# Optimization experiments

Hardware: AMD Instinct MI355X
Metric: run time of the kernel (lower is better)

Reference implementation:

```python
import jax, jax.numpy as jnp
import numpy as np

D_MODEL = 256   # per-head dim in this module
N_HEAD = 8
B, S = 4, 2048
NEG_INF = -1e9  # large negative in place of -inf for numerical safety


def setup_inputs() -> dict:
    key = jax.random.key(0)
    ks = jax.random.split(key, 8)
    d, h = D_MODEL, N_HEAD
    sc = 1.0 / np.sqrt(d)
    return {
        "Q": jax.random.normal(ks[0], (B, S, d), jnp.float32),
        "mask": jax.random.randint(ks[1], (B, S), 0, 2, jnp.int32),
        "WQ_w": jax.random.normal(ks[2], (h * d, d), jnp.float32) * sc,
        "WQ_b": jnp.zeros((h * d,), jnp.float32),
        "WK_w": jax.random.normal(ks[3], (h * d, d), jnp.float32) * sc,
        "WK_b": jnp.zeros((h * d,), jnp.float32),
        "WV_w": jax.random.normal(ks[4], (h * d, d), jnp.float32) * sc,
        "WV_b": jnp.zeros((h * d,), jnp.float32),
        "WO_w": jax.random.normal(ks[5], (d, h * d), jnp.float32) * sc,
        "WO_b": jnp.zeros((d,), jnp.float32),
        "ln_g": jnp.ones((d,), jnp.float32),
        "ln_b": jnp.zeros((d,), jnp.float32),
    }


def reference(Q, mask, WQ_w, WQ_b, WK_w, WK_b, WV_w, WV_b, WO_w, WO_b, ln_g, ln_b):
    b, s, d = Q.shape
    h = N_HEAD
    # projections (torch Linear: x @ W.T + b), split into heads: [b, h, s, d]
    q = (Q @ WQ_w.T + WQ_b).reshape(b, s, h, d).transpose(0, 2, 1, 3)
    k = (Q @ WK_w.T + WK_b).reshape(b, s, h, d).transpose(0, 2, 1, 3)
    v = (Q @ WV_w.T + WV_b).reshape(b, s, h, d).transpose(0, 2, 1, 3)
    # scaled dot-product scores [b, h, q, k]
    scores = jnp.einsum('bhqd,bhkd->bhqk', q, k) / jnp.sqrt(jnp.asarray(d, Q.dtype))
    key_mask = (mask != 0)[:, None, None, :]  # [b,1,1,k]
    scores = jnp.where(key_mask, scores, NEG_INF)
    alpha = jax.nn.softmax(scores, axis=-1)
    out = jnp.einsum('bhqk,bhkd->bhqd', alpha, v)
    out = out.transpose(0, 2, 1, 3).reshape(b, s, h * d)
    out = out @ WO_w.T + WO_b + Q  # dropout is identity in eval
    # LayerNorm over last dim
    mu = out.mean(-1, keepdims=True)
    var = out.var(-1, keepdims=True)
    return (out - mu) / jnp.sqrt(var + 1e-5) * ln_g + ln_b
```

## Files before the change

kernel.cpp:

```cpp
#include <hip/hip_runtime.h>
#include <cstddef>
#include <cstdint>

#define SQ 2048
#define DH 256
#define NH 8
#define BATCH 4
#define MROWS (BATCH*SQ)
#define HID (NH*DH)

typedef __attribute__((ext_vector_type(8)))  short bf16x8;
typedef __attribute__((ext_vector_type(16))) float f32x16;

typedef __attribute__((address_space(1))) const unsigned char gbuf_t;
typedef __attribute__((address_space(3))) unsigned char lbuf_t;

__device__ __forceinline__ void gl_lds16(const void* g, void* l) {
  __builtin_amdgcn_global_load_lds((gbuf_t*)g, (lbuf_t*)l, 16, 0, 0);
}

__device__ __forceinline__ unsigned short f2bf(float f) {
  unsigned u = __float_as_uint(f);
  unsigned r = (u + 0x7FFFu + ((u >> 16) & 1u)) >> 16;
  return (unsigned short)r;
}
__device__ __forceinline__ unsigned pk2(float a, float b) {
  return (unsigned)f2bf(a) | ((unsigned)f2bf(b) << 16);
}
__device__ __forceinline__ f32x16 zero16() {
  f32x16 v;
#pragma unroll
  for (int i = 0; i < 16; ++i) v[i] = 0.0f;
  return v;
}

__global__ void __launch_bounds__(256) cvt_kernel(
    const float* __restrict__ X,  const float* __restrict__ Wq,
    const float* __restrict__ Wk, const float* __restrict__ Wv,
    const float* __restrict__ Wo,
    unsigned short* __restrict__ Xb,  unsigned short* __restrict__ Wqb,
    unsigned short* __restrict__ Wkb, unsigned short* __restrict__ Wvb,
    unsigned short* __restrict__ Wob)
{
  int bid = blockIdx.x;
  const float* src; unsigned short* dst; size_t off;
  if      (bid < 512) { src = X;  dst = Xb;  off = (size_t)bid * 4096; }
  else if (bid < 640) { src = Wq; dst = Wqb; off = (size_t)(bid - 512) * 4096; }
  else if (bid < 768) { src = Wk; dst = Wkb; off = (size_t)(bid - 640) * 4096; }
  else if (bid < 896) { src = Wv; dst = Wvb; off = (size_t)(bid - 768) * 4096; }
  else                { src = Wo; dst = Wob; off = (size_t)(bid - 896) * 4096; }
  int tid = threadIdx.x;
#pragma unroll
  for (int k = 0; k < 4; ++k) {
    size_t idx = off + ((size_t)k * 256 + tid) * 4;
    float4 v = *(const float4*)(src + idx);
    uint2 o; o.x = pk2(v.x, v.y); o.y = pk2(v.z, v.w);
    *(uint2*)(dst + idx) = o;
  }
}

__global__ void __launch_bounds__(256) qkv_kernel(
    const unsigned short* __restrict__ Xbf,
    const unsigned short* __restrict__ Wqb,
    const unsigned short* __restrict__ Wkb,
    const unsigned short* __restrict__ Wvb,
    const float* __restrict__ bq, const float* __restrict__ bk, const float* __restrict__ bv,
    unsigned short* __restrict__ q_ws, unsigned short* __restrict__ k_ws,
    unsigned short* __restrict__ vt_ws)
{
  __shared__ unsigned char TA[65536];
  __shared__ unsigned char TB[65536];
  const int tid = threadIdx.x, w = tid >> 6, l = tid & 63;
  const int h = l >> 5, t = l & 31;
  const int wm = w >> 1, wn = w & 1;
  const int z = blockIdx.z;
  const int m0 = (z == 2) ? blockIdx.y * 128 : blockIdx.x * 128;
  const int n0 = (z == 2) ? blockIdx.x * 128 : blockIdx.y * 128;
  const unsigned short* Asrc = (z == 2) ? Wvb : Xbf;
  const unsigned short* Bsrc = (z == 0) ? Wqb : (z == 1) ? Wkb : Xbf;

  const int rowo = l >> 5;
  const int bin  = (l & 31) * 16;
#pragma unroll
  for (int i2 = 0; i2 < 16; ++i2) {
    int i = 16 * w + i2;
    int row = 2 * i + rowo;
    gl_lds16((const unsigned char*)(Asrc + (size_t)(m0 + row) * 256) + (bin ^ ((row & 15) << 4)),
             &TA[i * 1024]);
  }
#pragma unroll
  for (int i2 = 0; i2 < 16; ++i2) {
    int i = 16 * w + i2;
    int row = 2 * i + rowo;
    gl_lds16((const unsigned char*)(Bsrc + (size_t)(n0 + row) * 256) + (bin ^ ((row & 15) << 4)),
             &TB[i * 1024]);
  }
  __syncthreads();

  f32x16 acc00 = zero16(), acc01 = zero16(), acc10 = zero16(), acc11 = zero16();
  const int swz = (t & 15) << 4;
#pragma unroll
  for (int kc = 0; kc < 16; ++kc) {
    int kb = (32 * kc + 16 * h) ^ swz;
    bf16x8 a0 = *(const bf16x8*)&TA[(size_t)(64 * wm + t) * 512 + kb];
    bf16x8 a1 = *(const bf16x8*)&TA[(size_t)(64 * wm + 32 + t) * 512 + kb];
    bf16x8 b0 = *(const bf16x8*)&TB[(size_t)(64 * wn + t) * 512 + kb];
    bf16x8 b1 = *(const bf16x8*)&TB[(size_t)(64 * wn + 32 + t) * 512 + kb];
    acc00 = __builtin_amdgcn_mfma_f32_32x32x16_bf16(a0, b0, acc00, 0, 0, 0);
    acc01 = __builtin_amdgcn_mfma_f32_32x32x16_bf16(a0, b1, acc01, 0, 0, 0);
    acc10 = __builtin_amdgcn_mfma_f32_32x32x16_bf16(a1, b0, acc10, 0, 0, 0);
    acc11 = __builtin_amdgcn_mfma_f32_32x32x16_bf16(a1, b1, acc11, 0, 0, 0);
  }

  if (z < 2) {
    unsigned short* outp = z ? k_ws : q_ws;
    const float* bias = z ? bk : bq;
    float bn0 = bias[n0 + 64 * wn + t];
    float bn1 = bias[n0 + 64 * wn + 32 + t];
#pragma unroll
    for (int mt = 0; mt < 2; ++mt) {
#pragma unroll
      for (int nt = 0; nt < 2; ++nt) {
        int n = n0 + 64 * wn + 32 * nt + t;
        int headn = n >> 8, d = n & 255;
        float bb = nt ? bn1 : bn0;
        const f32x16& A = (mt == 0) ? (nt == 0 ? acc00 : acc01) : (nt == 0 ? acc10 : acc11);
#pragma unroll
        for (int r = 0; r < 16; ++r) {
          int m = m0 + 64 * wm + 32 * mt + (r & 3) + 8 * (r >> 2) + 4 * h;
          int batch = m >> 11, s = m & 2047;
          outp[(((size_t)batch * NH + headn) * SQ + s) * DH + d] = f2bf(A[r] + bb);
        }
      }
    }
  } else {
#pragma unroll
    for (int mt = 0; mt < 2; ++mt) {
#pragma unroll
      for (int r = 0; r < 16; ++r) {
        int j = m0 + 64 * wm + 32 * mt + (r & 3) + 8 * (r >> 2) + 4 * h;
        float bj = bv[j];
        int headj = j >> 8, jl = j & 255;
#pragma unroll
        for (int nt = 0; nt < 2; ++nt) {
          int sall = n0 + 64 * wn + 32 * nt + t;
          int batch = sall >> 11, ss = sall & 2047;
          const f32x16& A = (mt == 0) ? (nt == 0 ? acc00 : acc01) : (nt == 0 ? acc10 : acc11);
          vt_ws[((size_t)batch * NH + headj) * DH * SQ + (size_t)jl * SQ + ss] = f2bf(A[r] + bj);
        }
      }
    }
  }
}

__global__ void __launch_bounds__(512, 2) attn_kernel(
    const unsigned short* __restrict__ q_ws,
    const unsigned short* __restrict__ k_ws,
    const unsigned short* __restrict__ vt_ws,
    const int* __restrict__ mask,
    unsigned short* __restrict__ o_ws)
{
  __shared__ unsigned char KT[2][32768];
  __shared__ unsigned char VT[2][32768];
  __shared__ float MB[2048];

  const int tid = threadIdx.x, w = tid >> 6, l = tid & 63;
  const int h = l >> 5, t = l & 31;
  const int bid = blockIdx.x;
  const int xcd = bid & 7, slot = bid >> 3;
  const int bh = xcd * 4 + (slot >> 3);
  const int qt = slot & 7;
  const int b = bh >> 3, head = bh & 7;
  const int q0 = qt * 256;

  {
    const int* mrow = mask + b * SQ;
    for (int i = tid; i < SQ; i += 512) MB[i] = mrow[i] ? 0.0f : -1e9f;
  }

  const unsigned short* kplane = k_ws + (size_t)bh * SQ * DH;
  const unsigned short* vplane = vt_ws + (size_t)bh * DH * SQ;

  bf16x8 qf[16];
  {
    const unsigned short* qb = q_ws + ((size_t)bh * SQ + (q0 + 32 * w + t)) * DH + 8 * h;
#pragma unroll
    for (int kc = 0; kc < 16; ++kc) qf[kc] = *(const bf16x8*)(qb + 16 * kc);
  }

  const int krow_o = l >> 5, kcol = (l & 31) * 16;
  const int vrow_o = l >> 3, vcol = (l & 7) * 16;

  {
#pragma unroll
    for (int i = 0; i < 4; ++i) {
      int j = 4 * w + i;
      int row = 2 * j + krow_o;
      gl_lds16((const unsigned char*)(kplane + (size_t)row * DH) + (kcol ^ ((row & 15) << 4)),
               &KT[0][j * 1024]);
    }
#pragma unroll
    for (int i = 0; i < 4; ++i) {
      int j = 4 * w + i;
      int row = 8 * j + vrow_o;
      gl_lds16((const unsigned char*)(vplane + (size_t)row * SQ) + (vcol ^ ((row & 7) << 4)),
               &VT[0][j * 1024]);
    }
  }
  __syncthreads();

  f32x16 o[8];
#pragma unroll
  for (int i = 0; i < 8; ++i) o[i] = zero16();
  float m_run = -3.0e38f, l_run = 0.0f;

  const int swzK = (t & 15) << 4;
  const int swzV = (t & 7) << 4;

  int cur = 0;
  for (int kb = 0; kb < SQ; kb += 64) {
    const int nxt = cur ^ 1;
    if (kb + 64 < SQ) {
#pragma unroll
      for (int i = 0; i < 4; ++i) {
        int j = 4 * w + i;
        int row = 2 * j + krow_o;
        gl_lds16((const unsigned char*)(kplane + (size_t)(kb + 64 + row) * DH) + (kcol ^ ((row & 15) << 4)),
                 &KT[nxt][j * 1024]);
      }
#pragma unroll
      for (int i = 0; i < 4; ++i) {
        int j = 4 * w + i;
        int row = 8 * j + vrow_o;
        gl_lds16((const unsigned char*)(vplane + (size_t)row * SQ + kb + 64) + (vcol ^ ((row & 7) << 4)),
                 &VT[nxt][j * 1024]);
      }
    }

    f32x16 sa0 = zero16(), sa1 = zero16();
    __builtin_amdgcn_s_setprio(1);
#pragma unroll
    for (int kc = 0; kc < 16; ++kc) {
      int kbb = (32 * kc + 16 * h) ^ swzK;
      bf16x8 a0 = *(const bf16x8*)&KT[cur][(size_t)t * 512 + kbb];
      bf16x8 a1 = *(const bf16x8*)&KT[cur][(size_t)(32 + t) * 512 + kbb];
      sa0 = __builtin_amdgcn_mfma_f32_32x32x16_bf16(a0, qf[kc], sa0, 0, 0, 0);
      sa1 = __builtin_amdgcn_mfma_f32_32x32x16_bf16(a1, qf[kc], sa1, 0, 0, 0);
    }
    __builtin_amdgcn_s_setprio(0);

    float tm = -3.0e38f;
    const float* mbp = &MB[kb + 4 * h];
#pragma unroll
    for (int r = 0; r < 16; ++r) {
      int kl = (r & 3) + 8 * (r >> 2);
      sa0[r] = sa0[r] * 0.0625f + mbp[kl];
      sa1[r] = sa1[r] * 0.0625f + mbp[32 + kl];
      tm = fmaxf(tm, fmaxf(sa0[r], sa1[r]));
    }
    tm = fmaxf(tm, __shfl_xor(tm, 32, 64));
    float m_new = fmaxf(m_run, tm);
    float rf = __expf(m_run - m_new);
    m_run = m_new;
    float ls = 0.0f;
#pragma unroll
    for (int r = 0; r < 16; ++r) {
      sa0[r] = __expf(sa0[r] - m_new);
      sa1[r] = __expf(sa1[r] - m_new);
      ls += sa0[r] + sa1[r];
    }
    ls += __shfl_xor(ls, 32, 64);
    l_run = l_run * rf + ls;

#pragma unroll
    for (int r = 0; r < 16; ++r) {
      float rr = __shfl(rf, (r & 3) + 8 * (r >> 2) + 4 * h, 64);
#pragma unroll
      for (int db = 0; db < 8; ++db) o[db][r] *= rr;
    }

    bf16x8 pa[4];
#pragma unroll
    for (int ks = 0; ks < 4; ++ks) {
      const f32x16& P = (ks < 2) ? sa0 : sa1;
      const int base = 8 * (ks & 1);
      unsigned lo0 = pk2(P[base + 0], P[base + 1]);
      unsigned lo1 = pk2(P[base + 2], P[base + 3]);
      unsigned hi0 = pk2(P[base + 4], P[base + 5]);
      unsigned hi1 = pk2(P[base + 6], P[base + 7]);
      unsigned s0 = h ? lo0 : hi0;
      unsigned s1 = h ? lo1 : hi1;
      unsigned x0 = (unsigned)__shfl_xor((int)s0, 32, 64);
      unsigned x1 = (unsigned)__shfl_xor((int)s1, 32, 64);
      union { unsigned u[4]; bf16x8 v; } pu;
      pu.u[0] = h ? x0 : lo0;
      pu.u[1] = h ? x1 : lo1;
      pu.u[2] = h ? hi0 : x0;
      pu.u[3] = h ? hi1 : x1;
      pa[ks] = pu.v;
    }

    __builtin_amdgcn_s_setprio(1);
#pragma unroll
    for (int db = 0; db < 8; ++db) {
#pragma unroll
      for (int ks = 0; ks < 4; ++ks) {
        bf16x8 bv = *(const bf16x8*)&VT[cur][(size_t)(32 * db + t) * 128 + ((32 * ks + 16 * h) ^ swzV)];
        o[db] = __builtin_amdgcn_mfma_f32_32x32x16_bf16(pa[ks], bv, o[db], 0, 0, 0);
      }
    }
    __builtin_amdgcn_s_setprio(0);

    __syncthreads();
    cur = nxt;
  }

  float linv = 1.0f / l_run;
  unsigned short* ob = o_ws + (size_t)b * SQ * HID + (size_t)head * DH;
#pragma unroll
  for (int r = 0; r < 16; ++r) {
    int rowr = (r & 3) + 8 * (r >> 2) + 4 * h;
    float li = __shfl(linv, rowr, 64);
    int s = q0 + 32 * w + rowr;
    unsigned short* orow = ob + (size_t)s * HID;
#pragma unroll
    for (int db = 0; db < 8; ++db)
      orow[32 * db + t] = f2bf(o[db][r] * li);
  }
}

__global__ void __launch_bounds__(256) oproj_kernel(
    const unsigned short* __restrict__ Abf,
    const unsigned short* __restrict__ Wob,
    float* __restrict__ tmp)
{
  __shared__ unsigned char TA[8192];
  __shared__ unsigned char TB[16384];
  const int tid = threadIdx.x, w = tid >> 6, l = tid & 63;
  const int h = l >> 5, t = l & 31;
  const int wm = w >> 1, wn = w & 1;
  const int m0 = blockIdx.x * 64, n0 = blockIdx.y * 128;
  const int arow_o = l >> 3, ab_in = (l & 7) * 16;
  const int swz = (t & 7) << 4;

  f32x16 acc0 = zero16(), acc1 = zero16();
  for (int chunk = 0; chunk < 32; ++chunk) {
    __syncthreads();
#pragma unroll
    for (int i2 = 0; i2 < 2; ++i2) {
      int i = 2 * w + i2;
      int row = 8 * i + arow_o;
      gl_lds16((const unsigned char*)(Abf + (size_t)(m0 + row) * HID + chunk * 64) + (ab_in ^ ((row & 7) << 4)),
               &TA[i * 1024]);
    }
#pragma unroll
    for (int i2 = 0; i2 < 4; ++i2) {
      int i = 4 * w + i2;
      int row = 8 * i + arow_o;
      gl_lds16((const unsigned char*)(Wob + (size_t)(n0 + row) * HID + chunk * 64) + (ab_in ^ ((row & 7) << 4)),
               &TB[i * 1024]);
    }
    __syncthreads();
#pragma unroll
    for (int kc = 0; kc < 4; ++kc) {
      int kbb = (32 * kc + 16 * h) ^ swz;
      bf16x8 a  = *(const bf16x8*)&TA[(size_t)(32 * wm + t) * 128 + kbb];
      bf16x8 b0 = *(const bf16x8*)&TB[(size_t)(64 * wn + t) * 128 + kbb];
      bf16x8 b1 = *(const bf16x8*)&TB[(size_t)(64 * wn + 32 + t) * 128 + kbb];
      acc0 = __builtin_amdgcn_mfma_f32_32x32x16_bf16(a, b0, acc0, 0, 0, 0);
      acc1 = __builtin_amdgcn_mfma_f32_32x32x16_bf16(a, b1, acc1, 0, 0, 0);
    }
  }
#pragma unroll
  for (int nt = 0; nt < 2; ++nt) {
    const f32x16& A = nt ? acc1 : acc0;
    int n = n0 + 64 * wn + 32 * nt + t;
#pragma unroll
    for (int r = 0; r < 16; ++r) {
      int m = m0 + 32 * wm + (r & 3) + 8 * (r >> 2) + 4 * h;
      tmp[(size_t)m * DH + n] = A[r];
    }
  }
}

__global__ void __launch_bounds__(256) ln_kernel(
    const float* __restrict__ tmp, const float* __restrict__ bo,
    const float* __restrict__ Xin, const float* __restrict__ g,
    const float* __restrict__ be, float* __restrict__ out)
{
  const int tid = threadIdx.x, w = tid >> 6, lane = tid & 63;
  const int row = blockIdx.x * 4 + w;
  float4 v  = ((const float4*)(tmp + (size_t)row * DH))[lane];
  float4 qv = ((const float4*)(Xin + (size_t)row * DH))[lane];
  float4 bb = ((const float4*)bo)[lane];
  v.x += qv.x + bb.x; v.y += qv.y + bb.y; v.z += qv.z + bb.z; v.w += qv.w + bb.w;
  float s1 = v.x + v.y + v.z + v.w;
  float s2 = v.x * v.x + v.y * v.y + v.z * v.z + v.w * v.w;
#pragma unroll
  for (int off = 1; off < 64; off <<= 1) {
    s1 += __shfl_xor(s1, off, 64);
    s2 += __shfl_xor(s2, off, 64);
  }
  float mean = s1 * (1.0f / 256.0f);
  float var = s2 * (1.0f / 256.0f) - mean * mean;
  float rstd = rsqrtf(var + 1e-5f);
  float4 gg = ((const float4*)g)[lane];
  float4 b2 = ((const float4*)be)[lane];
  float4 o;
  o.x = (v.x - mean) * rstd * gg.x + b2.x;
  o.y = (v.y - mean) * rstd * gg.y + b2.y;
  o.z = (v.z - mean) * rstd * gg.z + b2.z;
  o.w = (v.w - mean) * rstd * gg.w + b2.w;
  ((float4*)(out + (size_t)row * DH))[lane] = o;
}

extern "C" void kernel_launch(void* const* d_in, const int* in_sizes, int n_in,
                              void* d_out, int out_size, void* d_ws, size_t ws_size,
                              hipStream_t stream) {
  const float* Q    = (const float*)d_in[0];
  const int*   mask = (const int*)  d_in[1];
  const float* WQ_w = (const float*)d_in[2];
  const float* WQ_b = (const float*)d_in[3];
  const float* WK_w = (const float*)d_in[4];
  const float* WK_b = (const float*)d_in[5];
  const float* WV_w = (const float*)d_in[6];
  const float* WV_b = (const float*)d_in[7];
  const float* WO_w = (const float*)d_in[8];
  const float* WO_b = (const float*)d_in[9];
  const float* ln_g = (const float*)d_in[10];
  const float* ln_b = (const float*)d_in[11];
  float* out = (float*)d_out;

  uint8_t* ws = (uint8_t*)d_ws;
  const size_t MB1 = 1048576;
  unsigned short* Xb   = (unsigned short*)(ws + 0 * MB1);
  unsigned short* Wqb  = (unsigned short*)(ws + 4 * MB1);
  unsigned short* Wkb  = (unsigned short*)(ws + 5 * MB1);
  unsigned short* Wvb  = (unsigned short*)(ws + 6 * MB1);
  unsigned short* Wob  = (unsigned short*)(ws + 7 * MB1);
  unsigned short* q_ws = (unsigned short*)(ws + 8 * MB1);
  unsigned short* k_ws = (unsigned short*)(ws + 40 * MB1);
  unsigned short* vtws = (unsigned short*)(ws + 72 * MB1);
  unsigned short* o_ws = (unsigned short*)(ws + 104 * MB1);
  float*          tmpf = (float*)         (ws + 136 * MB1);

  cvt_kernel<<<1024, 256, 0, stream>>>(Q, WQ_w, WK_w, WV_w, WO_w, Xb, Wqb, Wkb, Wvb, Wob);
  qkv_kernel<<<dim3(64, 16, 3), 256, 0, stream>>>(Xb, Wqb, Wkb, Wvb, WQ_b, WK_b, WV_b,
                                                  q_ws, k_ws, vtws);
  attn_kernel<<<dim3(256), 512, 0, stream>>>(q_ws, k_ws, vtws, mask, o_ws);
  oproj_kernel<<<dim3(128, 2), 256, 0, stream>>>(o_ws, Wob, tmpf);
  ln_kernel<<<2048, 256, 0, stream>>>(tmpf, WO_b, Q, ln_g, ln_b, out);
}
```

Measured before the change: 312.0 us.

## Use exp2 softmax with lazy rescaling, vectorized mask loads, and hardware bf16 packing

Folds log2(e) into the score scale so the softmax uses exp2f. The running-max update and the rescale of the output accumulator are skipped unless some lane's tile max exceeds the running max by a threshold. This removes the per-tile shuffle and multiply pass over 128 accumulator values in the common case. Mask bias is now read with float4 LDS loads, and P is packed to bf16 with the v_cvt_pk_bf16_f32 instruction instead of software rounding. The thresholded lazy max lets exponentials reach up to 2^11.5 before normalization, trading some numerical headroom for fewer rescale passes.

```diff
diff --git a/kernel.cpp b/kernel.cpp
--- a/kernel.cpp
+++ b/kernel.cpp
@@ -173,9 +173,12 @@
   const int b = bh >> 3, head = bh & 7;
   const int q0 = qt * 256;
 
+  const float SC2 = 0.0625f * 1.44269504f;
+  const float THR = 11.54f;
+
   {
     const int* mrow = mask + b * SQ;
-    for (int i = tid; i < SQ; i += 512) MB[i] = mrow[i] ? 0.0f : -1e9f;
+    for (int i = tid; i < SQ; i += 512) MB[i] = mrow[i] ? 0.0f : -1.0e9f;
   }
 
   const unsigned short* kplane = k_ws + (size_t)bh * SQ * DH;
@@ -249,45 +252,55 @@
     }
     __builtin_amdgcn_s_setprio(0);
 
+    float4 mb0[4], mb1[4];
+#pragma unroll
+    for (int g = 0; g < 4; ++g) {
+      mb0[g] = *(const float4*)&MB[kb + 4 * h + 8 * g];
+      mb1[g] = *(const float4*)&MB[kb + 32 + 4 * h + 8 * g];
+    }
     float tm = -3.0e38f;
-    const float* mbp = &MB[kb + 4 * h];
 #pragma unroll
     for (int r = 0; r < 16; ++r) {
-      int kl = (r & 3) + 8 * (r >> 2);
-      sa0[r] = sa0[r] * 0.0625f + mbp[kl];
-      sa1[r] = sa1[r] * 0.0625f + mbp[32 + kl];
-      tm = fmaxf(tm, fmaxf(sa0[r], sa1[r]));
+      int g = r >> 2, j = r & 3;
+      sa0[r] = sa0[r] * SC2 + ((const float*)&mb0[g])[j];
+      sa1[r] = sa1[r] * SC2 + ((const float*)&mb1[g])[j];
+      tm = fmaxf(fmaxf(tm, sa0[r]), sa1[r]);
     }
     tm = fmaxf(tm, __shfl_xor(tm, 32, 64));
-    float m_new = fmaxf(m_run, tm);
-    float rf = __expf(m_run - m_new);
-    m_run = m_new;
+
+    if (__builtin_expect(!__all(tm <= m_run + THR), 0)) {
+      float m_new = fmaxf(m_run, tm);
+      float rf = exp2f(m_run - m_new);
+      m_run = m_new;
+      l_run *= rf;
+#pragma unroll
+      for (int r = 0; r < 16; ++r) {
+        float rr = __shfl(rf, (r & 3) + 8 * (r >> 2) + 4 * h, 64);
+#pragma unroll
+        for (int db = 0; db < 8; ++db) o[db][r] *= rr;
+      }
+    }
+
     float ls = 0.0f;
 #pragma unroll
     for (int r = 0; r < 16; ++r) {
-      sa0[r] = __expf(sa0[r] - m_new);
-      sa1[r] = __expf(sa1[r] - m_new);
+      sa0[r] = exp2f(sa0[r] - m_run);
+      sa1[r] = exp2f(sa1[r] - m_run);
       ls += sa0[r] + sa1[r];
     }
     ls += __shfl_xor(ls, 32, 64);
-    l_run = l_run * rf + ls;
-
-#pragma unroll
-    for (int r = 0; r < 16; ++r) {
-      float rr = __shfl(rf, (r & 3) + 8 * (r >> 2) + 4 * h, 64);
-#pragma unroll
-      for (int db = 0; db < 8; ++db) o[db][r] *= rr;
-    }
+    l_run += ls;
 
     bf16x8 pa[4];
 #pragma unroll
     for (int ks = 0; ks < 4; ++ks) {
       const f32x16& P = (ks < 2) ? sa0 : sa1;
       const int base = 8 * (ks & 1);
-      unsigned lo0 = pk2(P[base + 0], P[base + 1]);
-      unsigned lo1 = pk2(P[base + 2], P[base + 3]);
-      unsigned hi0 = pk2(P[base + 4], P[base + 5]);
-      unsigned hi1 = pk2(P[base + 6], P[base + 7]);
+      unsigned lo0, lo1, hi0, hi1;
+      asm("v_cvt_pk_bf16_f32 %0, %1, %2" : "=v"(lo0) : "v"(P[base + 0]), "v"(P[base + 1]));
+      asm("v_cvt_pk_bf16_f32 %0, %1, %2" : "=v"(lo1) : "v"(P[base + 2]), "v"(P[base + 3]));
+      asm("v_cvt_pk_bf16_f32 %0, %1, %2" : "=v"(hi0) : "v"(P[base + 4]), "v"(P[base + 5]));
+      asm("v_cvt_pk_bf16_f32 %0, %1, %2" : "=v"(hi1) : "v"(P[base + 6]), "v"(P[base + 7]));
       unsigned s0 = h ? lo0 : hi0;
       unsigned s1 = h ? lo1 : hi1;
       unsigned x0 = (unsigned)__shfl_xor((int)s0, 32, 64);
```

Result: slower. 589.3 us (+88.9%).
